# Optimization experiments

Hardware: AMD Instinct MI355X
Metric: run time of the kernel (lower is better)

## Reference

```python
import jax, jax.numpy as jnp
import numpy as np

B, L, DM, NHEAD, DK, DV = 2, 2048, 1024, 16, 64, 64


def setup_inputs() -> dict:
    key = jax.random.key(0)
    ks = jax.random.split(key, 8)
    q = jax.random.normal(ks[0], (B, L, DM), dtype=jnp.float32)
    k = jax.random.normal(ks[1], (B, L, DM), dtype=jnp.float32)
    v = jax.random.normal(ks[2], (B, L, DM), dtype=jnp.float32)
    mask = jax.random.randint(ks[3], (B, L, L), 0, 2, dtype=jnp.int32)
    s = 1.0 / np.sqrt(DM)
    wq = jax.random.normal(ks[4], (DK * NHEAD, DM), dtype=jnp.float32) * s
    wk = jax.random.normal(ks[5], (DK * NHEAD, DM), dtype=jnp.float32) * s
    wv = jax.random.normal(ks[6], (DV * NHEAD, DM), dtype=jnp.float32) * s
    wo_w = jax.random.normal(ks[7], (DM, DV * NHEAD), dtype=jnp.float32) * s
    wo_b = jnp.zeros((DM,), dtype=jnp.float32)
    return {"q": q, "k": k, "v": v, "mask": mask,
            "wq": wq, "wk": wk, "wv": wv, "wo_w": wo_w, "wo_b": wo_b}


def reference(q, k, v, mask, wq, wk, wv, wo_w, wo_b):
    Bq, Lq, _ = q.shape
    Lk = k.shape[1]
    # linear projections, split into heads: (B, H, L, dk)
    qh = (q @ wq.T).reshape(Bq, Lq, NHEAD, DK).transpose(0, 2, 1, 3)
    kh = (k @ wk.T).reshape(Bq, Lk, NHEAD, DK).transpose(0, 2, 1, 3)
    vh = (v @ wv.T).reshape(Bq, Lk, NHEAD, DV).transpose(0, 2, 1, 3)
    scale = jnp.float32(1.0 / np.sqrt(DK))
    sim = jnp.einsum('bhqd,bhkd->bhqk', qh, kh) * scale
    # mask broadcast over heads (torch: mask.unsqueeze(1); fill -1e9 where mask==0)
    sim = jnp.where(mask[:, None, :, :] == 0, jnp.float32(-1e9), sim)
    attention = jax.nn.softmax(sim, axis=-1)  # dropout=0.0 -> identity
    context = jnp.einsum('bhqk,bhkd->bhqd', attention, vh)
    context = context.transpose(0, 2, 1, 3).reshape(Bq, Lq, DM)
    context = context @ wo_w.T + wo_b
    return (context, attention)
```

## Files before the change

### kernel.cpp

```cpp
#include <hip/hip_runtime.h>


typedef __attribute__((ext_vector_type(8))) short short8;
typedef __attribute__((ext_vector_type(4))) float f32x4;

#define MFMA_BF16(a,b,c) __builtin_amdgcn_mfma_f32_16x16x32_bf16((a),(b),(c),0,0,0)

__device__ __forceinline__ unsigned short f2bf(float f){
  union { float f; unsigned u; } x; x.f = f;
  unsigned r = (x.u + 0x7fffu + ((x.u >> 16) & 1u)) >> 16;
  return (unsigned short)r;
}
__device__ __forceinline__ float bf2f(unsigned short h){
  union { unsigned u; float f; } x; x.u = ((unsigned)h) << 16; return x.f;
}
__device__ __forceinline__ unsigned cvt_pk_bf16(float lo, float hi){
  unsigned r;
  asm("v_cvt_pk_bf16_f32 %0, %1, %2" : "=v"(r) : "v"(lo), "v"(hi));
  return r;
}

typedef __attribute__((address_space(1))) const void gas_void;
typedef __attribute__((address_space(3))) void las_void;
__device__ __forceinline__ void gload16(const void* g, void* l){
  __builtin_amdgcn_global_load_lds((gas_void*)g, (las_void*)l, 16, 0, 0);
}

__global__ __launch_bounds__(256) void prep_k(
    const float* __restrict__ q, const float* __restrict__ k,
    const float* __restrict__ v, const int* __restrict__ mask,
    const float* __restrict__ wq, const float* __restrict__ wk,
    const float* __restrict__ wv, const float* __restrict__ wo,
    unsigned short* __restrict__ qhi, unsigned short* __restrict__ qlo,
    unsigned short* __restrict__ khi, unsigned short* __restrict__ klo,
    unsigned short* __restrict__ vb,
    unsigned short* __restrict__ wqh, unsigned short* __restrict__ wql,
    unsigned short* __restrict__ wkh, unsigned short* __restrict__ wkl,
    unsigned short* __restrict__ wvb, unsigned short* __restrict__ wob_,
    unsigned long long* __restrict__ bits){
  const int blk = blockIdx.x;
  if (blk >= 16384){
    int mb = blk - 16384;
    int base = mb*1024 + (threadIdx.x >> 6)*256;
    int lane = threadIdx.x & 63;
#pragma unroll
    for (int j=0;j<4;j++){
      unsigned long long w = __ballot(mask[base + j*64 + lane] != 0);
      if (lane == 0) bits[(base >> 6) + j] = w;
    }
    return;
  }
  const float* src; unsigned short *hi, *lo; bool split; int i;
  if (blk < 12288){
    i = (blk & 4095)*256 + threadIdx.x;
    if (blk < 4096){ src=q; hi=qhi; lo=qlo; split=true; }
    else if (blk < 8192){ src=k; hi=khi; lo=klo; split=true; }
    else { src=v; hi=vb; lo=nullptr; split=false; }
  } else {
    i = (blk & 1023)*256 + threadIdx.x;
    int seg = (blk - 12288) >> 10;
    if (seg==0){ src=wq; hi=wqh; lo=wql; split=true; }
    else if (seg==1){ src=wk; hi=wkh; lo=wkl; split=true; }
    else if (seg==2){ src=wv; hi=wvb; lo=nullptr; split=false; }
    else { src=wo; hi=wob_; lo=nullptr; split=false; }
  }
  float4 f = reinterpret_cast<const float4*>(src)[i];
  ushort4 oh;
  oh.x=f2bf(f.x); oh.y=f2bf(f.y); oh.z=f2bf(f.z); oh.w=f2bf(f.w);
  reinterpret_cast<ushort4*>(hi)[i] = oh;
  if (split){
    ushort4 ol;
    ol.x=f2bf(f.x - bf2f(oh.x)); ol.y=f2bf(f.y - bf2f(oh.y));
    ol.z=f2bf(f.z - bf2f(oh.z)); ol.w=f2bf(f.w - bf2f(oh.w));
    reinterpret_cast<ushort4*>(lo)[i] = ol;
  }
}

__global__ __launch_bounds__(256,3) void proj_qkv_k(
    const unsigned short* __restrict__ qhi, const unsigned short* __restrict__ qlo,
    const unsigned short* __restrict__ khi, const unsigned short* __restrict__ klo,
    const unsigned short* __restrict__ vb,
    const unsigned short* __restrict__ wqh, const unsigned short* __restrict__ wql,
    const unsigned short* __restrict__ wkh, const unsigned short* __restrict__ wkl,
    const unsigned short* __restrict__ wvb,
    unsigned short* __restrict__ Qp, unsigned short* __restrict__ Kp,
    unsigned short* __restrict__ Vt){
  __shared__ __align__(16) char SA[2][8192];
  __shared__ __align__(16) char SB[2][8192];
  const int z = blockIdx.z;
  const unsigned short *A0, *A1, *W0, *W2;
  int nkt;
  if (z==0){ A0=qhi; A1=qlo; W0=wqh; W2=wql; nkt=96; }
  else if (z==1){ A0=khi; A1=klo; W0=wkh; W2=wkl; nkt=96; }
  else { A0=vb; A1=vb; W0=wvb; W2=wvb; nkt=32; }
  const int tid = threadIdx.x;
  const int wave = tid >> 6, lane = tid & 63;
  const int lr = lane & 15, lg = lane >> 4;
  const int m0 = blockIdx.y * 128, n0 = blockIdx.x * 128;
  const int wr = wave >> 1, wc = wave & 1;
  const f32x4 fz = {0.f,0.f,0.f,0.f};

  f32x4 acc[4][4];
#pragma unroll
  for (int i=0;i<4;i++)
#pragma unroll
    for (int j=0;j<4;j++) acc[i][j] = fz;

  auto stage = [&](int kt, int bu){
    int seg = kt >> 5;
    int kof = (kt & 31)*32 + (tid&3)*8;
    const unsigned short* A_ = (seg==1) ? A1 : A0;
    const unsigned short* W_ = (seg==2) ? W2 : W0;
#pragma unroll
    for (int i=0;i<2;i++){
      int row = i*64 + (tid>>2);
      int dof = i*4096 + wave*1024;
      gload16(A_ + (size_t)(m0+row)*1024 + kof, &SA[bu][dof]);
      gload16(W_ + (size_t)(n0+row)*1024 + kof, &SB[bu][dof]);
    }
  };
  stage(0,0);
  int buf = 0;
  for (int kt=0; kt<nkt; ++kt){
    __syncthreads();
    if (kt+1 < nkt) stage(kt+1, buf^1);
    short8 af[4], bf[4];
#pragma unroll
    for (int i=0;i<4;i++) af[i] = *(const short8*)(&SA[buf][(wr*64+i*16+lr)*64 + lg*16]);
#pragma unroll
    for (int j=0;j<4;j++) bf[j] = *(const short8*)(&SB[buf][(wc*64+j*16+lr)*64 + lg*16]);
#pragma unroll
    for (int i=0;i<4;i++)
#pragma unroll
      for (int j=0;j<4;j++)
        acc[i][j] = MFMA_BF16(af[i], bf[j], acc[i][j]);
    buf ^= 1;
  }

  if (z < 2){
    unsigned short* out = (z==0) ? Qp : Kp;
#pragma unroll
    for (int i=0;i<4;i++)
#pragma unroll
      for (int j=0;j<4;j++)
#pragma unroll
        for (int r=0;r<4;r++){
          int m = m0 + wr*64 + i*16 + lg*4 + r;
          int n = n0 + wc*64 + j*16 + lr;
          out[(size_t)m*1024 + n] = f2bf(acc[i][j][r]);
        }
  } else {
#pragma unroll
    for (int i=0;i<4;i++)
#pragma unroll
      for (int j=0;j<4;j++){
        int m = m0 + wr*64 + i*16 + lg*4;
        int n = n0 + wc*64 + j*16 + lr;
        int b = m >> 11, lrow = m & 2047;
        int h = n >> 6,  dv = n & 63;
        ushort4 o;
        o.x = f2bf(acc[i][j][0]); o.y = f2bf(acc[i][j][1]);
        o.z = f2bf(acc[i][j][2]); o.w = f2bf(acc[i][j][3]);
        *reinterpret_cast<ushort4*>(Vt + ((size_t)((b*16+h)*64+dv))*2048 + lrow) = o;
      }
  }
}

__global__ __launch_bounds__(256,3) void attn_pass1_k(
    const unsigned short* __restrict__ Qp, const unsigned short* __restrict__ Kp,
    const unsigned long long* __restrict__ mbits, float* __restrict__ linv){
  __shared__ __align__(16) char Ks[2][16384];
  const int tid = threadIdx.x;
  const int wave = tid >> 6, lane = tid & 63;
  const int lr = lane & 15, lg = lane >> 4;
  const int flat = blockIdx.x;
  const int wg = ((flat & 7) << 6) + (flat >> 3);
  const int bh = wg >> 4, b = bh >> 4, h = bh & 15;
  const int qbase = (wg & 15)*128 + wave*32;
  const f32x4 fz = {0.f,0.f,0.f,0.f};

  short8 qf[2][2];
#pragma unroll
  for (int ai=0;ai<2;ai++)
#pragma unroll
    for (int ks=0;ks<2;ks++)
      qf[ai][ks] = *(const short8*)(Qp + (size_t)(b*2048 + qbase + ai*16 + lr)*1024
                                    + h*64 + ks*32 + lg*8);
  float psum[2] = {0.f, 0.f};

  auto stageK = [&](int t, int bu){
#pragma unroll
    for (int i=0;i<4;i++){
      int byte = i*4096 + tid*16;
      int row = byte >> 7;
      int ch  = (byte >> 4) & 7;
      gload16(Kp + (size_t)(b*2048 + t*128 + row)*1024 + h*64 + ((ch ^ (row&7))*8),
              &Ks[bu][i*4096 + wave*1024]);
    }
  };
  stageK(0,0);
  int buf = 0;
  for (int t=0; t<16; ++t){
    __syncthreads();
    if (t+1 < 16) stageK(t+1, buf^1);
    f32x4 s2[2][8];
#pragma unroll
    for (int ai=0;ai<2;ai++)
#pragma unroll
      for (int bj=0;bj<8;bj++) s2[ai][bj] = fz;
#pragma unroll
    for (int ks=0;ks<2;ks++){
      short8 kf[8];
#pragma unroll
      for (int bj=0;bj<8;bj++){
        int row = bj*16 + lr;
        kf[bj] = *(const short8*)(&Ks[buf][row*128 + (((ks*4+lg) ^ (row&7))*16)]);
      }
#pragma unroll
      for (int ai=0;ai<2;ai++)
#pragma unroll
        for (int bj=0;bj<8;bj++)
          s2[ai][bj] = MFMA_BF16(kf[bj], qf[ai][ks], s2[ai][bj]);
    }
#pragma unroll
    for (int ai=0;ai<2;ai++){
      int qrow = qbase + ai*16 + lr;
      ulonglong2 mw = *reinterpret_cast<const ulonglong2*>(
          mbits + (((size_t)(b*2048 + qrow)) << 5) + t*2);
      unsigned long long wx = mw.x >> (lg*4);
      unsigned long long wy = mw.y >> (lg*4);
      float a0 = 0.f;
#pragma unroll
      for (int bj=0;bj<8;bj++){
        unsigned ub = (unsigned)(((bj<4) ? wx : wy) >> ((bj&3)*16));
#pragma unroll
        for (int r=0;r<4;r++){
          float e = __expf(s2[ai][bj][r]*0.125f);
          a0 += (ub & (1u<<r)) ? e : 0.f;
        }
      }
      psum[ai] += a0;
    }
    buf ^= 1;
  }
#pragma unroll
  for (int ai=0;ai<2;ai++){
    float v = psum[ai];
    v += __shfl_xor(v, 16, 64);
    v += __shfl_xor(v, 32, 64);
    if (lg == 0)
      linv[(size_t)bh*2048 + qbase + ai*16 + lr] = 1.f / v;
  }
}

__global__ __launch_bounds__(256,4) void attn_pass2_k(
    const unsigned short* __restrict__ Qp, const unsigned short* __restrict__ Kp,
    const unsigned short* __restrict__ Vt, const unsigned long long* __restrict__ mbits,
    const float* __restrict__ linv, float* __restrict__ attn,
    unsigned short* __restrict__ ctx){
  __shared__ __align__(16) char Ks[2][8192];
  __shared__ __align__(16) char Vs[2][8192];
  __shared__ __align__(16) unsigned short Ps[64*64];
  const int tid = threadIdx.x;
  const int wave = tid >> 6, lane = tid & 63;
  const int lr = lane & 15, lg = lane >> 4;
  const int flat = blockIdx.x;
  const int wg = ((flat & 7) << 7) + (flat >> 3);
  const int bh = wg >> 5, b = bh >> 4, h = bh & 15;
  const int qbase = (wg & 31)*64 + wave*16;
  const f32x4 fz = {0.f,0.f,0.f,0.f};

  short8 qf[2];
#pragma unroll
  for (int ks=0;ks<2;ks++)
    qf[ks] = *(const short8*)(Qp + (size_t)(b*2048 + qbase + lr)*1024
                              + h*64 + ks*32 + lg*8);
  const int qrow = qbase + lr;
  const float li = linv[(size_t)bh*2048 + qrow];
  const unsigned long long* mrow = mbits + (((size_t)(b*2048 + qrow)) << 5);

  f32x4 oacc[4];
#pragma unroll
  for (int bj=0;bj<4;bj++) oacc[bj] = fz;

  auto stageK = [&](int t, int bu){
#pragma unroll
    for (int i=0;i<2;i++){
      int byte = i*4096 + tid*16;
      int row = byte >> 7;
      int ch  = (byte >> 4) & 7;
      gload16(Kp + (size_t)(b*2048 + t*64 + row)*1024 + h*64 + ((ch ^ (row&7))*8),
              &Ks[bu][i*4096 + wave*1024]);
    }
  };
  auto stageV = [&](int t, int bu){
#pragma unroll
    for (int i=0;i<2;i++){
      int byte = i*4096 + tid*16;
      int row = byte >> 7;
      int ch  = (byte >> 4) & 7;
      gload16(Vt + (size_t)(bh*64 + row)*2048 + t*64 + ((ch ^ (row&7))*8),
              &Vs[bu][i*4096 + wave*1024]);
    }
  };
  auto wload = [&](int t) -> unsigned long long {
    unsigned long long wv;
    const unsigned long long* ma = mrow + t;
    asm volatile("global_load_dwordx2 %0, %1, off" : "=v"(wv) : "v"(ma));
    return wv;
  };

  stageK(0,0); stageV(0,0);
  unsigned long long w_cur = wload(0), w_nxt = 0;
  asm volatile("s_waitcnt vmcnt(0)" ::: "memory");
  __builtin_amdgcn_s_barrier();

  char* psb = (char*)Ps;
  const int prow = (wave*16 + lr);
  const int pswz = (lr & 7) << 4;
  const int rl = lane >> 4, c = lane & 15;
  float* attnW = attn + ((size_t)bh*2048 + qbase)*2048 + c*4;
  int buf = 0;
  for (int t=0; t<32; ++t){
    if (t+1 < 32){ stageK(t+1, buf^1); stageV(t+1, buf^1); w_nxt = wload(t+1); }
    __builtin_amdgcn_sched_barrier(0);

    f32x4 s2[4];
#pragma unroll
    for (int bj=0;bj<4;bj++) s2[bj] = fz;
#pragma unroll
    for (int ks=0;ks<2;ks++){
      short8 kf[4];
#pragma unroll
      for (int bj=0;bj<4;bj++){
        int row = bj*16 + lr;
        kf[bj] = *(const short8*)(&Ks[buf][row*128 + (((ks*4+lg) ^ (row&7))*16)]);
      }
#pragma unroll
      for (int bj=0;bj<4;bj++)
        s2[bj] = MFMA_BF16(kf[bj], qf[ks], s2[bj]);
    }
    unsigned long long w2 = w_cur >> (lg*4);
#pragma unroll
    for (int bj=0;bj<4;bj++){
      unsigned ub = (unsigned)(w2 >> (bj*16));
      f32x4 po;
#pragma unroll
      for (int r=0;r<4;r++){
        float e = __expf(s2[bj][r]*0.125f);
        po[r] = (ub & (1u<<r)) ? e*li : 0.f;
      }
      uint2 pk;
      pk.x = cvt_pk_bf16(po[0], po[1]);
      pk.y = cvt_pk_bf16(po[2], po[3]);
      *reinterpret_cast<uint2*>(psb + prow*128 + (((bj*32 + lg*8) ^ pswz))) = pk;
    }
    __builtin_amdgcn_sched_barrier(0);
    asm volatile("s_waitcnt lgkmcnt(0)" ::: "memory");
    __builtin_amdgcn_sched_barrier(0);
#pragma unroll
    for (int rg=0; rg<4; ++rg){
      int R = rg*4 + rl;
      const char* src = psb + (wave*16 + R)*128 + ((c*8) ^ ((R&7)<<4));
      uint2 d = *reinterpret_cast<const uint2*>(src);
      union { unsigned u; float f; } c0, c1, c2, c3;
      c0.u = d.x << 16; c1.u = d.x & 0xffff0000u;
      c2.u = d.y << 16; c3.u = d.y & 0xffff0000u;
      f32x4 po2 = { c0.f, c1.f, c2.f, c3.f };
      __builtin_nontemporal_store(po2,
          reinterpret_cast<f32x4*>(attnW + (size_t)R*2048 + t*64));
    }
#pragma unroll
    for (int ks=0;ks<2;ks++){
      short8 pa = *(const short8*)(psb + prow*128 + (((ks*64 + lg*16) ^ pswz)));
      short8 vf[4];
#pragma unroll
      for (int bj=0;bj<4;bj++){
        int row = bj*16 + lr;
        vf[bj] = *(const short8*)(&Vs[buf][row*128 + (((ks*4+lg) ^ (row&7))*16)]);
      }
#pragma unroll
      for (int bj=0;bj<4;bj++)
        oacc[bj] = MFMA_BF16(pa, vf[bj], oacc[bj]);
    }
    if (t+1 < 32){
      __builtin_amdgcn_sched_barrier(0);
      asm volatile("s_waitcnt vmcnt(4)" ::: "memory");
      asm volatile("s_waitcnt lgkmcnt(0)" ::: "memory");
      __builtin_amdgcn_s_barrier();
    }
    w_cur = w_nxt;
    buf ^= 1;
  }
#pragma unroll
  for (int bj=0;bj<4;bj++)
#pragma unroll
    for (int r=0;r<4;r++){
      int qr2 = qbase + lg*4 + r;
      int dv = bj*16 + lr;
      ctx[(size_t)(b*2048 + qr2)*1024 + h*64 + dv] = f2bf(oacc[bj][r]);
    }
}

__global__ __launch_bounds__(256,4) void gemm_out_k(const unsigned short* __restrict__ A,
    const unsigned short* __restrict__ W, float* __restrict__ out,
    const float* __restrict__ bias){
  __shared__ __align__(16) char As[2][4096];
  __shared__ __align__(16) char Bs[2][8192];
  const int tid = threadIdx.x;
  const int wave = tid >> 6, lane = tid & 63;
  const int lr = lane & 15, lg = lane >> 4;
  const int m0 = blockIdx.y * 64, n0 = blockIdx.x * 128;
  const int wr = wave >> 1, wc = wave & 1;
  const f32x4 fz = {0.f,0.f,0.f,0.f};

  f32x4 acc[2][4];
#pragma unroll
  for (int i=0;i<2;i++)
#pragma unroll
    for (int j=0;j<4;j++) acc[i][j] = fz;

  auto stage = [&](int kt, int bu){
    int kof = kt*32 + (tid&3)*8;
    gload16(A + (size_t)(m0 + (tid>>2))*1024 + kof, &As[bu][wave*1024]);
#pragma unroll
    for (int i=0;i<2;i++){
      int row = i*64 + (tid>>2);
      gload16(W + (size_t)(n0+row)*1024 + kof, &Bs[bu][i*4096 + wave*1024]);
    }
  };
  stage(0,0);
  int buf = 0;
  for (int kt=0; kt<32; ++kt){
    __syncthreads();
    if (kt+1 < 32) stage(kt+1, buf^1);
    short8 af[2], bf[4];
#pragma unroll
    for (int i=0;i<2;i++) af[i] = *(const short8*)(&As[buf][(wr*32+i*16+lr)*64 + lg*16]);
#pragma unroll
    for (int j=0;j<4;j++) bf[j] = *(const short8*)(&Bs[buf][(wc*64+j*16+lr)*64 + lg*16]);
#pragma unroll
    for (int i=0;i<2;i++)
#pragma unroll
      for (int j=0;j<4;j++)
        acc[i][j] = MFMA_BF16(af[i], bf[j], acc[i][j]);
    buf ^= 1;
  }
#pragma unroll
  for (int i=0;i<2;i++)
#pragma unroll
    for (int j=0;j<4;j++){
      int n = n0 + wc*64 + j*16 + lr;
      float bv = bias[n];
#pragma unroll
      for (int r=0;r<4;r++){
        int m = m0 + wr*32 + i*16 + lg*4 + r;
        out[(size_t)m*1024 + n] = acc[i][j][r] + bv;
      }
    }
}

extern "C" void kernel_launch(void* const* d_in, const int* in_sizes, int n_in,
                              void* d_out, int out_size, void* d_ws, size_t ws_size,
                              hipStream_t stream){
  (void)in_sizes; (void)n_in; (void)out_size;
  const float* q   = (const float*)d_in[0];
  const float* k   = (const float*)d_in[1];
  const float* v   = (const float*)d_in[2];
  const int*  mask = (const int*)d_in[3];
  const float* wq  = (const float*)d_in[4];
  const float* wk  = (const float*)d_in[5];
  const float* wv  = (const float*)d_in[6];
  const float* wo  = (const float*)d_in[7];
  const float* wob = (const float*)d_in[8];

  char* ws = (char*)d_ws;
  const size_t MB = 1ull << 20;
  unsigned short* qhi = (unsigned short*)(ws +  0*MB);
  unsigned short* qlo = (unsigned short*)(ws +  8*MB);
  unsigned short* khi = (unsigned short*)(ws + 16*MB);
  unsigned short* klo = (unsigned short*)(ws + 24*MB);
  unsigned short* vb  = (unsigned short*)(ws + 32*MB);
  unsigned short* wqh = (unsigned short*)(ws + 40*MB);
  unsigned short* wql = (unsigned short*)(ws + 42*MB);
  unsigned short* wkh = (unsigned short*)(ws + 44*MB);
  unsigned short* wkl = (unsigned short*)(ws + 46*MB);
  unsigned short* wvb = (unsigned short*)(ws + 48*MB);
  unsigned short* wob_= (unsigned short*)(ws + 50*MB);
  unsigned short* Qp  = (unsigned short*)(ws + 52*MB);
  unsigned short* Kp  = (unsigned short*)(ws + 60*MB);
  unsigned short* Vt  = (unsigned short*)(ws + 68*MB);
  unsigned short* Ctx = (unsigned short*)(ws + 76*MB);
  unsigned long long* mbits = (unsigned long long*)(ws + 84*MB);
  float*          lin = (float*)(ws + 0*MB);
  if (ws_size < 85*MB) return;

  float* ctx_out  = (float*)d_out;
  float* attn_out = ctx_out + (size_t)2*2048*1024;

  prep_k<<<24576,256,0,stream>>>(q,k,v,mask,wq,wk,wv,wo,
                                 qhi,qlo,khi,klo,vb,
                                 wqh,wql,wkh,wkl,wvb,wob_, mbits);

  proj_qkv_k<<<dim3(8,32,3),256,0,stream>>>(qhi,qlo,khi,klo,vb,
                                            wqh,wql,wkh,wkl,wvb, Qp,Kp,Vt);

  attn_pass1_k<<<512,256,0,stream>>>(Qp, Kp, mbits, lin);
  attn_pass2_k<<<1024,256,0,stream>>>(Qp, Kp, Vt, mbits, lin,
                                      attn_out, Ctx);

  gemm_out_k<<<dim3(8,64),256,0,stream>>>(Ctx, wob_, ctx_out, wob);
}
```

Measured before the change: 295.8 us.

## Double query rows per wave in attention pass2 to reuse K/V tiles

Each wave in the second attention pass now handles 32 query rows (two 16-row MFMA tiles) instead of 16, so a workgroup covers 128 queries and the grid is halved. Each K and V tile staged in shared memory is reused across twice as many rows, which halves global K/V staging traffic and barrier count per query. The cost is more registers (launch bounds lowered to 2 blocks), a larger P buffer in LDS, and fewer workgroups, which reduces occupancy for a kernel that is largely bound by writing the attention matrix.

```diff
diff --git a/kernel.cpp b/kernel.cpp
--- a/kernel.cpp
+++ b/kernel.cpp
@@ -253,35 +253,44 @@
   }
 }
 
-__global__ __launch_bounds__(256,4) void attn_pass2_k(
+__global__ __launch_bounds__(256,2) void attn_pass2_k(
     const unsigned short* __restrict__ Qp, const unsigned short* __restrict__ Kp,
     const unsigned short* __restrict__ Vt, const unsigned long long* __restrict__ mbits,
     const float* __restrict__ linv, float* __restrict__ attn,
     unsigned short* __restrict__ ctx){
   __shared__ __align__(16) char Ks[2][8192];
   __shared__ __align__(16) char Vs[2][8192];
-  __shared__ __align__(16) unsigned short Ps[64*64];
+  __shared__ __align__(16) unsigned short Ps[128*64];
   const int tid = threadIdx.x;
   const int wave = tid >> 6, lane = tid & 63;
   const int lr = lane & 15, lg = lane >> 4;
   const int flat = blockIdx.x;
-  const int wg = ((flat & 7) << 7) + (flat >> 3);
-  const int bh = wg >> 5, b = bh >> 4, h = bh & 15;
-  const int qbase = (wg & 31)*64 + wave*16;
+  const int wg = ((flat & 7) << 6) + (flat >> 3);
+  const int bh = wg >> 4, b = bh >> 4, h = bh & 15;
+  const int qbase = (wg & 15)*128 + wave*32;
   const f32x4 fz = {0.f,0.f,0.f,0.f};
 
-  short8 qf[2];
-#pragma unroll
-  for (int ks=0;ks<2;ks++)
-    qf[ks] = *(const short8*)(Qp + (size_t)(b*2048 + qbase + lr)*1024
-                              + h*64 + ks*32 + lg*8);
-  const int qrow = qbase + lr;
-  const float li = linv[(size_t)bh*2048 + qrow];
-  const unsigned long long* mrow = mbits + (((size_t)(b*2048 + qrow)) << 5);
-
-  f32x4 oacc[4];
-#pragma unroll
-  for (int bj=0;bj<4;bj++) oacc[bj] = fz;
+  short8 qf[2][2];
+#pragma unroll
+  for (int ai=0;ai<2;ai++)
+#pragma unroll
+    for (int ks=0;ks<2;ks++)
+      qf[ai][ks] = *(const short8*)(Qp + (size_t)(b*2048 + qbase + ai*16 + lr)*1024
+                                    + h*64 + ks*32 + lg*8);
+  float li[2];
+  const unsigned long long* mrow[2];
+#pragma unroll
+  for (int ai=0;ai<2;ai++){
+    int qrow = qbase + ai*16 + lr;
+    li[ai] = linv[(size_t)bh*2048 + qrow];
+    mrow[ai] = mbits + (((size_t)(b*2048 + qrow)) << 5);
+  }
+
+  f32x4 oacc[2][4];
+#pragma unroll
+  for (int ai=0;ai<2;ai++)
+#pragma unroll
+    for (int bj=0;bj<4;bj++) oacc[ai][bj] = fz;
 
   auto stageK = [&](int t, int bu){
 #pragma unroll
@@ -303,31 +312,36 @@
               &Vs[bu][i*4096 + wave*1024]);
     }
   };
-  auto wload = [&](int t) -> unsigned long long {
+  auto wload = [&](int ai, int t) -> unsigned long long {
     unsigned long long wv;
-    const unsigned long long* ma = mrow + t;
+    const unsigned long long* ma = mrow[ai] + t;
     asm volatile("global_load_dwordx2 %0, %1, off" : "=v"(wv) : "v"(ma));
     return wv;
   };
 
   stageK(0,0); stageV(0,0);
-  unsigned long long w_cur = wload(0), w_nxt = 0;
+  unsigned long long w_cur0 = wload(0,0), w_cur1 = wload(1,0);
+  unsigned long long w_nxt0 = 0, w_nxt1 = 0;
   asm volatile("s_waitcnt vmcnt(0)" ::: "memory");
   __builtin_amdgcn_s_barrier();
 
   char* psb = (char*)Ps;
-  const int prow = (wave*16 + lr);
   const int pswz = (lr & 7) << 4;
   const int rl = lane >> 4, c = lane & 15;
   float* attnW = attn + ((size_t)bh*2048 + qbase)*2048 + c*4;
   int buf = 0;
   for (int t=0; t<32; ++t){
-    if (t+1 < 32){ stageK(t+1, buf^1); stageV(t+1, buf^1); w_nxt = wload(t+1); }
+    if (t+1 < 32){
+      stageK(t+1, buf^1); stageV(t+1, buf^1);
+      w_nxt0 = wload(0, t+1); w_nxt1 = wload(1, t+1);
+    }
     __builtin_amdgcn_sched_barrier(0);
 
-    f32x4 s2[4];
-#pragma unroll
-    for (int bj=0;bj<4;bj++) s2[bj] = fz;
+    f32x4 s2[2][4];
+#pragma unroll
+    for (int ai=0;ai<2;ai++)
+#pragma unroll
+      for (int bj=0;bj<4;bj++) s2[ai][bj] = fz;
 #pragma unroll
     for (int ks=0;ks<2;ks++){
       short8 kf[4];
@@ -337,31 +351,37 @@
         kf[bj] = *(const short8*)(&Ks[buf][row*128 + (((ks*4+lg) ^ (row&7))*16)]);
       }
 #pragma unroll
-      for (int bj=0;bj<4;bj++)
-        s2[bj] = MFMA_BF16(kf[bj], qf[ks], s2[bj]);
-    }
-    unsigned long long w2 = w_cur >> (lg*4);
-#pragma unroll
-    for (int bj=0;bj<4;bj++){
-      unsigned ub = (unsigned)(w2 >> (bj*16));
-      f32x4 po;
-#pragma unroll
-      for (int r=0;r<4;r++){
-        float e = __expf(s2[bj][r]*0.125f);
-        po[r] = (ub & (1u<<r)) ? e*li : 0.f;
-      }
-      uint2 pk;
-      pk.x = cvt_pk_bf16(po[0], po[1]);
-      pk.y = cvt_pk_bf16(po[2], po[3]);
-      *reinterpret_cast<uint2*>(psb + prow*128 + (((bj*32 + lg*8) ^ pswz))) = pk;
+      for (int ai=0;ai<2;ai++)
+#pragma unroll
+        for (int bj=0;bj<4;bj++)
+          s2[ai][bj] = MFMA_BF16(kf[bj], qf[ai][ks], s2[ai][bj]);
+    }
+#pragma unroll
+    for (int ai=0;ai<2;ai++){
+      unsigned long long w2 = ((ai==0) ? w_cur0 : w_cur1) >> (lg*4);
+      int prow = wave*32 + ai*16 + lr;
+#pragma unroll
+      for (int bj=0;bj<4;bj++){
+        unsigned ub = (unsigned)(w2 >> (bj*16));
+        f32x4 po;
+#pragma unroll
+        for (int r=0;r<4;r++){
+          float e = __expf(s2[ai][bj][r]*0.125f);
+          po[r] = (ub & (1u<<r)) ? e*li[ai] : 0.f;
+        }
+        uint2 pk;
+        pk.x = cvt_pk_bf16(po[0], po[1]);
+        pk.y = cvt_pk_bf16(po[2], po[3]);
+        *reinterpret_cast<uint2*>(psb + prow*128 + (((bj*32 + lg*8) ^ pswz))) = pk;
+      }
     }
     __builtin_amdgcn_sched_barrier(0);
     asm volatile("s_waitcnt lgkmcnt(0)" ::: "memory");
     __builtin_amdgcn_sched_barrier(0);
 #pragma unroll
-    for (int rg=0; rg<4; ++rg){
+    for (int rg=0; rg<8; ++rg){
       int R = rg*4 + rl;
-      const char* src = psb + (wave*16 + R)*128 + ((c*8) ^ ((R&7)<<4));
+      const char* src = psb + (wave*32 + R)*128 + ((c*8) ^ ((R&7)<<4));
       uint2 d = *reinterpret_cast<const uint2*>(src);
       union { unsigned u; float f; } c0, c1, c2, c3;
       c0.u = d.x << 16; c1.u = d.x & 0xffff0000u;
@@ -372,7 +392,12 @@
     }
 #pragma unroll
     for (int ks=0;ks<2;ks++){
-      short8 pa = *(const short8*)(psb + prow*128 + (((ks*64 + lg*16) ^ pswz)));
+      short8 pa[2];
+#pragma unroll
+      for (int ai=0;ai<2;ai++){
+        int prow = wave*32 + ai*16 + lr;
+        pa[ai] = *(const short8*)(psb + prow*128 + (((ks*64 + lg*16) ^ pswz)));
+      }
       short8 vf[4];
 #pragma unroll
       for (int bj=0;bj<4;bj++){
@@ -380,26 +405,30 @@
         vf[bj] = *(const short8*)(&Vs[buf][row*128 + (((ks*4+lg) ^ (row&7))*16)]);
       }
 #pragma unroll
-      for (int bj=0;bj<4;bj++)
-        oacc[bj] = MFMA_BF16(pa, vf[bj], oacc[bj]);
+      for (int ai=0;ai<2;ai++)
+#pragma unroll
+        for (int bj=0;bj<4;bj++)
+          oacc[ai][bj] = MFMA_BF16(pa[ai], vf[bj], oacc[ai][bj]);
     }
     if (t+1 < 32){
       __builtin_amdgcn_sched_barrier(0);
-      asm volatile("s_waitcnt vmcnt(4)" ::: "memory");
+      asm volatile("s_waitcnt vmcnt(8)" ::: "memory");
       asm volatile("s_waitcnt lgkmcnt(0)" ::: "memory");
       __builtin_amdgcn_s_barrier();
     }
-    w_cur = w_nxt;
+    w_cur0 = w_nxt0; w_cur1 = w_nxt1;
     buf ^= 1;
   }
 #pragma unroll
-  for (int bj=0;bj<4;bj++)
-#pragma unroll
-    for (int r=0;r<4;r++){
-      int qr2 = qbase + lg*4 + r;
-      int dv = bj*16 + lr;
-      ctx[(size_t)(b*2048 + qr2)*1024 + h*64 + dv] = f2bf(oacc[bj][r]);
-    }
+  for (int ai=0;ai<2;ai++)
+#pragma unroll
+    for (int bj=0;bj<4;bj++)
+#pragma unroll
+      for (int r=0;r<4;r++){
+        int qr2 = qbase + ai*16 + lg*4 + r;
+        int dv = bj*16 + lr;
+        ctx[(size_t)(b*2048 + qr2)*1024 + h*64 + dv] = f2bf(oacc[ai][bj][r]);
+      }
 }
 
 __global__ __launch_bounds__(256,4) void gemm_out_k(const unsigned short* __restrict__ A,
@@ -506,8 +535,8 @@
                                             wqh,wql,wkh,wkl,wvb, Qp,Kp,Vt);
 
   attn_pass1_k<<<512,256,0,stream>>>(Qp, Kp, mbits, lin);
-  attn_pass2_k<<<1024,256,0,stream>>>(Qp, Kp, Vt, mbits, lin,
-                                      attn_out, Ctx);
+  attn_pass2_k<<<512,256,0,stream>>>(Qp, Kp, Vt, mbits, lin,
+                                     attn_out, Ctx);
 
   gemm_out_k<<<dim3(8,64),256,0,stream>>>(Ctx, wob_, ctx_out, wob);
 }
```

Result: slower. 308.0 us (+4.1%).
